# Performance work log

Measured on AMD Instinct MI355X. Metric: run time of the kernel, lower is better.

The kernel has to match this reference:

```python
import jax, jax.numpy as jnp
import numpy as np

TT_IPS = (8, 16, 16)
TT_OPS = (16, 16, 16)
TT_RANKS = (1, 32, 32, 1)
BATCH = 4096


def setup_inputs() -> dict:
    key = jax.random.key(0)
    ks = jax.random.split(key, 6)
    ip0, ip1, ip2 = TT_IPS
    op0, op1, op2 = TT_OPS
    r1, r2 = TT_RANKS[1], TT_RANKS[2]
    # keras 'uniform' initializer: U(-0.05, 0.05)
    u = lambda k, s: jax.random.uniform(k, s, jnp.float32, -0.05, 0.05)
    return {
        "x": jax.random.normal(ks[0], (BATCH, ip0, ip1, ip2), jnp.float32),
        "core0": u(ks[1], (ip0, op0, r1)),
        "core1": u(ks[2], (r1, ip1, op1, r2)),
        "core2": u(ks[3], (r2, ip2, op2)),
        "bias": u(ks[4], (op0, op1, op2)),
    }


def reference(x, core0, core1, core2, bias):
    # Reconstruct dense weight via TT-core tensordot chain (as in the original).
    # core0: (i0, o0, r1); core1: (r1, i1, o1, r2); core2: (r2, i2, o2)
    w = jnp.tensordot(core0, core1, axes=[[-1], [0]])   # (i0, o0, i1, o1, r2)
    w = jnp.tensordot(w, core2, axes=[[-1], [0]])        # (i0, o0, i1, o1, i2, o2)
    # Contract input dims (1,2,3) of x with input dims (0,2,4) of w.
    out = jnp.tensordot(x, w, axes=[[1, 2, 3], [0, 2, 4]])  # (B, o0, o1, o2)
    return out + bias
```

## Files before the change

### kernel.cpp

```cpp
#include <hip/hip_runtime.h>
#include <hip/hip_bf16.h>
#include <stdint.h>


#define BATCH 4096
#define KIN   2048
#define NOUT  4096

typedef __bf16 bf16x8 __attribute__((ext_vector_type(8)));
typedef float  f32x4  __attribute__((ext_vector_type(4)));

__device__ __forceinline__ unsigned short f32_to_bf16_rne(float f) {
    union { float f; uint32_t u; } v; v.f = f;
    uint32_t u = v.u;
    u += 0x7fffu + ((u >> 16) & 1u);
    return (unsigned short)(u >> 16);
}

__global__ __launch_bounds__(256) void build_w01(
    const float* __restrict__ core0,
    const float* __restrict__ core1,
    float* __restrict__ w01)
{
    __shared__ float c0L[32 * 32];
    __shared__ float c1L[32 * 256];

    const int tid = threadIdx.x;
    const int r0  = blockIdx.y * 32;
    const int c0  = blockIdx.x * 256;

    *(f32x4*)&c0L[tid * 4] = *(const f32x4*)&core0[r0 * 32 + tid * 4];
#pragma unroll
    for (int i = 0; i < 8; ++i) {
        int idx = tid + i * 256;
        int r1  = idx >> 6;
        int cq  = idx & 63;
        *(f32x4*)&c1L[idx * 4] =
            *(const f32x4*)&core1[(size_t)r1 * 8192 + c0 + cq * 4];
    }
    __syncthreads();

    float acc[32];
#pragma unroll
    for (int r = 0; r < 32; ++r) acc[r] = 0.f;

#pragma unroll
    for (int q = 0; q < 8; ++q) {
        float cv0 = c1L[(4 * q + 0) * 256 + tid];
        float cv1 = c1L[(4 * q + 1) * 256 + tid];
        float cv2 = c1L[(4 * q + 2) * 256 + tid];
        float cv3 = c1L[(4 * q + 3) * 256 + tid];
#pragma unroll
        for (int r = 0; r < 32; ++r) {
            f32x4 w4 = *(const f32x4*)&c0L[r * 32 + q * 4];
            acc[r] += w4.x * cv0 + w4.y * cv1 + w4.z * cv2 + w4.w * cv3;
        }
    }

#pragma unroll
    for (int r = 0; r < 32; ++r)
        w01[(size_t)(r0 + r) * 8192 + c0 + tid] = acc[r];
}

__global__ __launch_bounds__(256) void build_wt(
    const float* __restrict__ w01,
    const float* __restrict__ core2,
    unsigned short* __restrict__ wt)
{
    __shared__ float w01L[32 * 32];
    __shared__ float c2p[32 * 256];

    const int tid = threadIdx.x;
    const int rb  = blockIdx.x * 32;

    *(f32x4*)&w01L[tid * 4] = *(const f32x4*)&w01[(size_t)rb * 32 + tid * 4];
#pragma unroll
    for (int i = 0; i < 8; ++i) {
        int fidx = tid + i * 256;
        int r2   = fidx >> 6;
        int cq   = fidx & 63;
        f32x4 v = *(const f32x4*)&core2[r2 * 256 + cq * 4];
#pragma unroll
        for (int j = 0; j < 4; ++j) {
            int cc = cq * 4 + j;
            int pc = (cc & 15) * 16 + (cc >> 4);
            c2p[r2 * 256 + pc] = v[j];
        }
    }
    __syncthreads();

    float acc[32];
#pragma unroll
    for (int r = 0; r < 32; ++r) acc[r] = 0.f;

#pragma unroll
    for (int q = 0; q < 8; ++q) {
        float cv0 = c2p[(4 * q + 0) * 256 + tid];
        float cv1 = c2p[(4 * q + 1) * 256 + tid];
        float cv2 = c2p[(4 * q + 2) * 256 + tid];
        float cv3 = c2p[(4 * q + 3) * 256 + tid];
#pragma unroll
        for (int r = 0; r < 32; ++r) {
            f32x4 w4 = *(const f32x4*)&w01L[r * 32 + q * 4];
            acc[r] += w4.x * cv0 + w4.y * cv1 + w4.z * cv2 + w4.w * cv3;
        }
    }

    const int i1base = (rb >> 4) & 15;
    const int o0     = (rb >> 8) & 15;
    const int i0     = rb >> 12;
    const int n0     = o0 * 256;
    const int k0     = i0 * 256 + i1base * 16;
    const int o2     = tid >> 4;
    const int i2     = tid & 15;

#pragma unroll
    for (int r = 0; r < 32; ++r) {
        int n = n0 + (r & 15) * 16 + o2;
        int k = k0 + (r >> 4) * 16 + i2;
        wt[(size_t)n * KIN + k] = f32_to_bf16_rne(acc[r]);
    }
}

__global__ __launch_bounds__(256) void cvt_x(
    const float* __restrict__ x,
    unsigned short* __restrict__ x2)
{
    int g4 = blockIdx.x * blockDim.x + threadIdx.x;
    f32x4 v = *(const f32x4*)&x[(size_t)g4 * 4];
    ushort4 h;
    h.x = f32_to_bf16_rne(v.x);
    h.y = f32_to_bf16_rne(v.y);
    h.z = f32_to_bf16_rne(v.z);
    h.w = f32_to_bf16_rne(v.w);
    *(ushort4*)&x2[(size_t)g4 * 4] = h;
}

__global__ __launch_bounds__(256, 2) void tt_gemm(
    const unsigned short* __restrict__ x2,
    const unsigned short* __restrict__ wt,
    const float* __restrict__ bias,
    float* __restrict__ out)
{
    __shared__ __align__(16) unsigned short lds_a[128 * 32];
    __shared__ __align__(16) unsigned short lds_b[128 * 32];

    const int tid  = threadIdx.x;
    const int lane = tid & 63;
    const int wid  = tid >> 6;
    const int wr   = wid >> 1;
    const int wc   = wid & 1;
    const int m0   = blockIdx.y * 128;
    const int n0   = blockIdx.x * 128;

    f32x4 acc[4][4] = {};

    const int seg0 = wid * 2 * 64 + lane;
    const int row0 = seg0 >> 2;
    const int cs0  = (seg0 & 3) * 8;
    const int seg1 = seg0 + 64;
    const int row1 = seg1 >> 2;
    const int cs1  = (seg1 & 3) * 8;

    for (int k0 = 0; k0 < KIN; k0 += 32) {
        const unsigned short* ga0 = x2 + (size_t)(m0 + row0) * KIN + k0 + cs0;
        const unsigned short* ga1 = x2 + (size_t)(m0 + row1) * KIN + k0 + cs1;
        const unsigned short* gb0 = wt + (size_t)(n0 + row0) * KIN + k0 + cs0;
        const unsigned short* gb1 = wt + (size_t)(n0 + row1) * KIN + k0 + cs1;

        __builtin_amdgcn_global_load_lds(
            (const __attribute__((address_space(1))) uint32_t*)ga0,
            (__attribute__((address_space(3))) uint32_t*)&lds_a[(wid * 2 + 0) * 512],
            16, 0, 0);
        __builtin_amdgcn_global_load_lds(
            (const __attribute__((address_space(1))) uint32_t*)ga1,
            (__attribute__((address_space(3))) uint32_t*)&lds_a[(wid * 2 + 1) * 512],
            16, 0, 0);
        __builtin_amdgcn_global_load_lds(
            (const __attribute__((address_space(1))) uint32_t*)gb0,
            (__attribute__((address_space(3))) uint32_t*)&lds_b[(wid * 2 + 0) * 512],
            16, 0, 0);
        __builtin_amdgcn_global_load_lds(
            (const __attribute__((address_space(1))) uint32_t*)gb1,
            (__attribute__((address_space(3))) uint32_t*)&lds_b[(wid * 2 + 1) * 512],
            16, 0, 0);

        __syncthreads();

        bf16x8 af[4], bf[4];
#pragma unroll
        for (int m = 0; m < 4; ++m)
            af[m] = *(const bf16x8*)&lds_a[(wr * 64 + m * 16 + (lane & 15)) * 32 + (lane >> 4) * 8];
#pragma unroll
        for (int n = 0; n < 4; ++n)
            bf[n] = *(const bf16x8*)&lds_b[(wc * 64 + n * 16 + (lane & 15)) * 32 + (lane >> 4) * 8];

#pragma unroll
        for (int m = 0; m < 4; ++m)
#pragma unroll
            for (int n = 0; n < 4; ++n)
                acc[m][n] = __builtin_amdgcn_mfma_f32_16x16x32_bf16(af[m], bf[n], acc[m][n], 0, 0, 0);

        __syncthreads();
    }

    const int colb = n0 + wc * 64 + (lane & 15);
#pragma unroll
    for (int n = 0; n < 4; ++n) {
        float bv = bias[colb + n * 16];
#pragma unroll
        for (int m = 0; m < 4; ++m) {
            int rbase = m0 + wr * 64 + m * 16 + (lane >> 4) * 4;
            f32x4 v = acc[m][n];
#pragma unroll
            for (int r = 0; r < 4; ++r)
                out[(size_t)(rbase + r) * NOUT + colb + n * 16] = v[r] + bv;
        }
    }
}

extern "C" void kernel_launch(void* const* d_in, const int* in_sizes, int n_in,
                              void* d_out, int out_size, void* d_ws, size_t ws_size,
                              hipStream_t stream) {
    const float* x     = (const float*)d_in[0];
    const float* core0 = (const float*)d_in[1];
    const float* core1 = (const float*)d_in[2];
    const float* core2 = (const float*)d_in[3];
    const float* bias  = (const float*)d_in[4];
    float* out = (float*)d_out;

    char* ws = (char*)d_ws;
    float*          w01 = (float*)ws;
    unsigned short* wt  = (unsigned short*)(ws + (4u << 20));
    unsigned short* x2  = (unsigned short*)(ws + (20u << 20));

    build_w01<<<dim3(32, 4), 256, 0, stream>>>(core0, core1, w01);
    build_wt <<<1024, 256, 0, stream>>>(w01, core2, wt);
    cvt_x    <<<8192, 256, 0, stream>>>(x, x2);
    tt_gemm  <<<dim3(32, 32), 256, 0, stream>>>(x2, wt, bias, out);
}
```

Before: 194.6 us.

## Fuse weight reconstruction and x conversion into one prep kernel

Result: faster. 185.3 us (-4.8%).

```diff
diff --git a/kernel.cpp b/kernel.cpp
--- a/kernel.cpp
+++ b/kernel.cpp
@@ -17,63 +17,50 @@
     return (unsigned short)(u >> 16);
 }
 
-__global__ __launch_bounds__(256) void build_w01(
+__global__ __launch_bounds__(256) void prep(
+    const float* __restrict__ x,
     const float* __restrict__ core0,
     const float* __restrict__ core1,
-    float* __restrict__ w01)
-{
-    __shared__ float c0L[32 * 32];
-    __shared__ float c1L[32 * 256];
-
-    const int tid = threadIdx.x;
-    const int r0  = blockIdx.y * 32;
-    const int c0  = blockIdx.x * 256;
-
-    *(f32x4*)&c0L[tid * 4] = *(const f32x4*)&core0[r0 * 32 + tid * 4];
-#pragma unroll
-    for (int i = 0; i < 8; ++i) {
-        int idx = tid + i * 256;
-        int r1  = idx >> 6;
-        int cq  = idx & 63;
-        *(f32x4*)&c1L[idx * 4] =
-            *(const f32x4*)&core1[(size_t)r1 * 8192 + c0 + cq * 4];
-    }
-    __syncthreads();
-
-    float acc[32];
-#pragma unroll
-    for (int r = 0; r < 32; ++r) acc[r] = 0.f;
-
-#pragma unroll
-    for (int q = 0; q < 8; ++q) {
-        float cv0 = c1L[(4 * q + 0) * 256 + tid];
-        float cv1 = c1L[(4 * q + 1) * 256 + tid];
-        float cv2 = c1L[(4 * q + 2) * 256 + tid];
-        float cv3 = c1L[(4 * q + 3) * 256 + tid];
-#pragma unroll
-        for (int r = 0; r < 32; ++r) {
-            f32x4 w4 = *(const f32x4*)&c0L[r * 32 + q * 4];
-            acc[r] += w4.x * cv0 + w4.y * cv1 + w4.z * cv2 + w4.w * cv3;
-        }
-    }
-
-#pragma unroll
-    for (int r = 0; r < 32; ++r)
-        w01[(size_t)(r0 + r) * 8192 + c0 + tid] = acc[r];
-}
-
-__global__ __launch_bounds__(256) void build_wt(
-    const float* __restrict__ w01,
     const float* __restrict__ core2,
+    unsigned short* __restrict__ x2,
     unsigned short* __restrict__ wt)
 {
     __shared__ float w01L[32 * 32];
     __shared__ float c2p[32 * 256];
 
     const int tid = threadIdx.x;
-    const int rb  = blockIdx.x * 32;
-
-    *(f32x4*)&w01L[tid * 4] = *(const f32x4*)&w01[(size_t)rb * 32 + tid * 4];
+    const int blk = blockIdx.x;
+
+    if (blk < 8192) {
+        int g4 = blk * 256 + tid;
+        f32x4 v = *(const f32x4*)&x[(size_t)g4 * 4];
+        ushort4 h;
+        h.x = f32_to_bf16_rne(v.x);
+        h.y = f32_to_bf16_rne(v.y);
+        h.z = f32_to_bf16_rne(v.z);
+        h.w = f32_to_bf16_rne(v.w);
+        *(ushort4*)&x2[(size_t)g4 * 4] = h;
+        return;
+    }
+
+    const int b  = blk - 8192;
+    const int rb = b * 32;
+    const int row2  = rb >> 8;
+    const int cbase = (rb & 255) * 32;
+
+    {
+        f32x4 acc4 = {0.f, 0.f, 0.f, 0.f};
+        const float* c1p = core1 + cbase + tid * 4;
+        const float* c0p = core0 + row2 * 32;
+#pragma unroll
+        for (int r1 = 0; r1 < 32; ++r1) {
+            float a  = c0p[r1];
+            f32x4 cv = *(const f32x4*)&c1p[(size_t)r1 * 8192];
+            acc4 += a * cv;
+        }
+        *(f32x4*)&w01L[tid * 4] = acc4;
+    }
+
 #pragma unroll
     for (int i = 0; i < 8; ++i) {
         int fidx = tid + i * 256;
@@ -120,20 +107,6 @@
         int k = k0 + (r >> 4) * 16 + i2;
         wt[(size_t)n * KIN + k] = f32_to_bf16_rne(acc[r]);
     }
-}
-
-__global__ __launch_bounds__(256) void cvt_x(
-    const float* __restrict__ x,
-    unsigned short* __restrict__ x2)
-{
-    int g4 = blockIdx.x * blockDim.x + threadIdx.x;
-    f32x4 v = *(const f32x4*)&x[(size_t)g4 * 4];
-    ushort4 h;
-    h.x = f32_to_bf16_rne(v.x);
-    h.y = f32_to_bf16_rne(v.y);
-    h.z = f32_to_bf16_rne(v.z);
-    h.w = f32_to_bf16_rne(v.w);
-    *(ushort4*)&x2[(size_t)g4 * 4] = h;
 }
 
 __global__ __launch_bounds__(256, 2) void tt_gemm(
@@ -230,12 +203,9 @@
     float* out = (float*)d_out;
 
     char* ws = (char*)d_ws;
-    float*          w01 = (float*)ws;
-    unsigned short* wt  = (unsigned short*)(ws + (4u << 20));
-    unsigned short* x2  = (unsigned short*)(ws + (20u << 20));
-
-    build_w01<<<dim3(32, 4), 256, 0, stream>>>(core0, core1, w01);
-    build_wt <<<1024, 256, 0, stream>>>(w01, core2, wt);
-    cvt_x    <<<8192, 256, 0, stream>>>(x, x2);
-    tt_gemm  <<<dim3(32, 32), 256, 0, stream>>>(x2, wt, bias, out);
-}
+    unsigned short* wt = (unsigned short*)ws;
+    unsigned short* x2 = (unsigned short*)(ws + (16u << 20));
+
+    prep   <<<8192 + 1024, 256, 0, stream>>>(x, core0, core1, core2, x2, wt);
+    tt_gemm<<<dim3(32, 32), 256, 0, stream>>>(x2, wt, bias, out);
+}
```
